# Kernel optimization log

Hardware: AMD Instinct MI355X
Metric: run time of the kernel (lower is better)

Reference implementation:

```python
import jax, jax.numpy as jnp
import numpy as np

D = 768
B = 32
N = 768


def setup_inputs() -> dict:
    key = jax.random.key(0)
    k1, k2, k3, k4 = jax.random.split(key, 4)
    stdv = 1.0 / np.sqrt(D)
    X = jax.random.normal(k1, (B, N, D), dtype=jnp.float32)
    adj = jax.random.uniform(k2, (B, N, N), dtype=jnp.float32)
    W_l = jax.random.uniform(k3, (D, D), dtype=jnp.float32, minval=-stdv, maxval=stdv)
    W_l1 = jax.random.uniform(k4, (D, D), dtype=jnp.float32, minval=-stdv, maxval=stdv)
    return {"X": X, "adj": adj, "W_l": W_l, "W_l1": W_l1}


def _row_normalize(adj):
    # rowsum^-1 with inf -> 0 (rows summing to zero stay zero)
    rowsum = adj.sum(axis=-1, keepdims=True)  # [B, N, 1]
    r_inv = jnp.where(rowsum == 0, 0.0, 1.0 / rowsum)
    return adj * r_inv


def reference(X, adj, W_l, W_l1):
    # X: [B, N, D], adj: [B, N, N]
    adj_n = _row_normalize(adj)
    e1 = jnp.einsum('bnd,de->bne', X, W_l1)        # message transform
    e11 = jnp.einsum('bnm,bmd->bnd', adj_n, e1)    # aggregate
    X1 = jnp.einsum('bnd,de->bne', X, W_l)         # self transform
    h = X1 + e11
    return jax.nn.leaky_relu(h, negative_slope=0.01)
```

## Files before the change

kernel.cpp:

```cpp
#include <hip/hip_runtime.h>
#include <hip/hip_bf16.h>
#include <cstdint>
#include <cstddef>

#define BN_ROWS 24576
#define DD 768
#define BE (768*768)
#define BM 384
#define BN_T 192
#define BK 32
#define ABUF 24576
#define BUFSZ 36864

typedef __attribute__((ext_vector_type(8))) short bf16x8;
typedef __attribute__((ext_vector_type(4))) float f32x4;

static __device__ __forceinline__ unsigned short f2bf(float f) {
  unsigned int u = __builtin_bit_cast(unsigned int, f);
  unsigned int lsb = (u >> 16) & 1u;
  u += 0x7fffu + lsb;
  return (unsigned short)(u >> 16);
}


__global__ __launch_bounds__(256) void convertX(const float* __restrict__ x,
                                                unsigned short* __restrict__ xb, int n4) {
  int idx = blockIdx.x * blockDim.x + threadIdx.x;
  int stride = gridDim.x * blockDim.x;
  for (int i = idx; i < n4; i += stride) {
    float4 v = reinterpret_cast<const float4*>(x)[i];
    ushort4 o;
    o.x = f2bf(v.x); o.y = f2bf(v.y); o.z = f2bf(v.z); o.w = f2bf(v.w);
    reinterpret_cast<ushort4*>(xb)[i] = o;
  }
}

__global__ __launch_bounds__(256) void convertWT(const float* __restrict__ Wl,
                                                 const float* __restrict__ Wl1,
                                                 unsigned short* __restrict__ WlT,
                                                 unsigned short* __restrict__ Wl1T) {
  __shared__ float tile[64][65];
  int tr = blockIdx.x / 12, tc = blockIdx.x % 12;
  int c = threadIdx.x & 63, r0 = threadIdx.x >> 6;
  const float* srcs[2] = {Wl, Wl1};
  unsigned short* dsts[2] = {WlT, Wl1T};
  #pragma unroll
  for (int m = 0; m < 2; ++m) {
    const float* src = srcs[m];
    #pragma unroll
    for (int i = 0; i < 16; ++i) {
      int r = r0 + i * 4;
      tile[r][c] = src[(size_t)(tr * 64 + r) * DD + tc * 64 + c];
    }
    __syncthreads();
    unsigned short* dst = dsts[m];
    #pragma unroll
    for (int i = 0; i < 16; ++i) {
      int r2 = r0 + i * 4;
      dst[(size_t)(tc * 64 + r2) * DD + tr * 64 + c] = f2bf(tile[c][r2]);
    }
    __syncthreads();
  }
}

__global__ __launch_bounds__(256) void adjNorm(const float* __restrict__ adj,
                                               unsigned short* __restrict__ adjnb) {
  int wid = threadIdx.x >> 6, lane = threadIdx.x & 63;
  int row = blockIdx.x * 4 + wid;
  const float4* a = reinterpret_cast<const float4*>(adj + (size_t)row * DD);
  float4 v[3];
  float s = 0.f;
  #pragma unroll
  for (int i = 0; i < 3; ++i) {
    v[i] = a[i * 64 + lane];
    s += (v[i].x + v[i].y) + (v[i].z + v[i].w);
  }
  #pragma unroll
  for (int off = 32; off; off >>= 1) s += __shfl_down(s, off);
  s = __shfl(s, 0);
  float rinv = (s == 0.f) ? 0.f : 1.f / s;
  ushort4* o = reinterpret_cast<ushort4*>(adjnb + (size_t)row * DD);
  #pragma unroll
  for (int i = 0; i < 3; ++i) {
    ushort4 u;
    u.x = f2bf(v[i].x * rinv); u.y = f2bf(v[i].y * rinv);
    u.z = f2bf(v[i].z * rinv); u.w = f2bf(v[i].w * rinv);
    o[i * 64 + lane] = u;
  }
}


template<int MODE>
__global__ __launch_bounds__(512, 2) void gemm8(
    const unsigned short* __restrict__ P0,
    const unsigned short* __restrict__ P1,
    const unsigned short* __restrict__ P2,
    const unsigned short* __restrict__ P3,
    void* __restrict__ outp)
{
  __shared__ char smem[3 * BUFSZ];
  constexpr int NT = MODE ? 48 : 24;
  const int tid = threadIdx.x, lane = tid & 63;
  const int wid = tid >> 6, wr = wid >> 1, wc = wid & 1;

  const int logical = (blockIdx.x & 7) * 32 + (blockIdx.x >> 3);

  const unsigned short *Ab0, *Bb0, *Ab1 = nullptr, *Bb1 = nullptr;
  int mt, nt, b;
  if (MODE == 0) {
    mt = logical >> 2; nt = logical & 3;
    b = mt >> 1;
    Ab0 = P0 + (size_t)mt * BM * DD;
    Bb0 = P1 + (size_t)nt * BN_T * DD;
  } else {
    b = logical >> 3; int r = logical & 7; mt = r >> 2; nt = r & 3;
    size_t bo = (size_t)b * BE;
    Ab0 = P0 + bo + (size_t)mt * BM * DD;
    Bb0 = P1 + bo + (size_t)nt * BN_T * DD;
    Ab1 = P2 + bo + (size_t)mt * BM * DD;
    Bb1 = P3 + (size_t)nt * BN_T * DD;
  }

  const int r_in = lane >> 2;
  const int s_in = lane & 3;

  auto stage = [&](int s) {
    int sc = s < NT ? s : 0;
    const int buf = (s % 3) * BUFSZ;
    const unsigned short *Abase, *Bbase;
    int kk;
    if (MODE == 1 && sc >= 24) { kk = sc - 24; Abase = Ab1; Bbase = Bb1; }
    else                       { kk = sc;      Abase = Ab0; Bbase = Bb0; }
    if (wid < 4) {
      #pragma unroll
      for (int i = 0; i < 6; ++i) {
        int row = wid * 96 + i * 16 + r_in;
        int slot = s_in ^ ((row >> 1) & 3);
        const unsigned short* src = Abase + (size_t)row * DD + kk * BK + slot * 8;
        __builtin_amdgcn_global_load_lds(
            (const __attribute__((address_space(1))) void*)src,
            (__attribute__((address_space(3))) void*)(smem + buf + (wid * 96 + i * 16) * 64),
            16, 0, 0);
      }
    } else {
      #pragma unroll
      for (int i = 0; i < 3; ++i) {
        int row = (wid - 4) * 48 + i * 16 + r_in;
        int slot = s_in ^ ((row >> 1) & 3);
        const unsigned short* src = Bbase + (size_t)row * DD + kk * BK + slot * 8;
        __builtin_amdgcn_global_load_lds(
            (const __attribute__((address_space(1))) void*)src,
            (__attribute__((address_space(3))) void*)(smem + buf + ABUF + ((wid - 4) * 48 + i * 16) * 64),
            16, 0, 0);
      }
    }
  };

  const int ks = lane >> 4;
  auto frag = [&](int off, int row) -> bf16x8 {
    int slot = ks ^ ((row >> 1) & 3);
    return *reinterpret_cast<const bf16x8*>(smem + off + row * 64 + slot * 16);
  };

  f32x4 acc[6][6] = {};

  stage(0); stage(1);

  for (int t = 0; t < NT; ++t) {
    stage(t + 2);
    if (wid < 4) asm volatile("s_waitcnt vmcnt(12)" ::: "memory");
    else         asm volatile("s_waitcnt vmcnt(6)"  ::: "memory");
    __builtin_amdgcn_s_barrier();

    const int bufA = (t % 3) * BUFSZ;
    const int bufB = bufA + ABUF;
    bf16x8 af[6], bg[6];
    #pragma unroll
    for (int i = 0; i < 6; ++i) {
      af[i] = frag(bufA, wr * 96 + i * 16 + (lane & 15));
      bg[i] = frag(bufB, wc * 96 + i * 16 + (lane & 15));
    }
    __builtin_amdgcn_s_setprio(1);
    #pragma unroll
    for (int mi = 0; mi < 6; ++mi)
      #pragma unroll
      for (int ni = 0; ni < 6; ++ni)
        acc[mi][ni] = __builtin_amdgcn_mfma_f32_16x16x32_bf16(af[mi], bg[ni], acc[mi][ni], 0, 0, 0);
    __builtin_amdgcn_s_setprio(0);
    __builtin_amdgcn_s_barrier();
  }

  if (MODE == 0) {
    unsigned short* ob = (unsigned short*)outp + (size_t)b * BE;
    const int mloc = (mt & 1) * BM + wr * 96 + (lane >> 4) * 4;
    #pragma unroll
    for (int mi = 0; mi < 6; ++mi)
      #pragma unroll
      for (int ni = 0; ni < 6; ++ni) {
        int m = mloc + mi * 16;
        int d = nt * BN_T + wc * 96 + ni * 16 + (lane & 15);
        f32x4 v = acc[mi][ni];
        ushort4 o;
        o.x = f2bf(v[0]); o.y = f2bf(v[1]); o.z = f2bf(v[2]); o.w = f2bf(v[3]);
        *reinterpret_cast<ushort4*>(ob + (size_t)d * DD + m) = o;
      }
  } else {
    float* ob = (float*)outp + (size_t)b * BE;
    const int mloc = mt * BM + wr * 96 + (lane >> 4) * 4;
    #pragma unroll
    for (int mi = 0; mi < 6; ++mi)
      #pragma unroll
      for (int ni = 0; ni < 6; ++ni) {
        int m = mloc + mi * 16;
        int n = nt * BN_T + wc * 96 + ni * 16 + (lane & 15);
        f32x4 v = acc[mi][ni];
        #pragma unroll
        for (int j = 0; j < 4; ++j) {
          float x = v[j];
          ob[(size_t)(m + j) * DD + n] = x > 0.f ? x : 0.01f * x;
        }
      }
  }
}


extern "C" void kernel_launch(void* const* d_in, const int* in_sizes, int n_in,
                              void* d_out, int out_size, void* d_ws, size_t ws_size,
                              hipStream_t stream) {
  const float* X   = (const float*)d_in[0];
  const float* adj = (const float*)d_in[1];
  const float* Wl  = (const float*)d_in[2];
  const float* Wl1 = (const float*)d_in[3];
  float* out = (float*)d_out;

  char* ws = (char*)d_ws;
  const size_t SZ = (size_t)BN_ROWS * DD * 2;
  unsigned short* Xb    = (unsigned short*)(ws);
  unsigned short* adjnb = (unsigned short*)(ws + SZ);
  unsigned short* e1T   = (unsigned short*)(ws + 2 * SZ);
  unsigned short* WlT   = (unsigned short*)(ws + 3 * SZ);
  unsigned short* Wl1T  = (unsigned short*)(ws + 3 * SZ + (size_t)BE * 2);

  convertX<<<4096, 256, 0, stream>>>(X, Xb, (BN_ROWS * DD) / 4);
  convertWT<<<144, 256, 0, stream>>>(Wl, Wl1, WlT, Wl1T);
  adjNorm<<<BN_ROWS / 4, 256, 0, stream>>>(adj, adjnb);
  gemm8<0><<<256, 512, 0, stream>>>(Xb, Wl1T, nullptr, nullptr, e1T);
  gemm8<1><<<256, 512, 0, stream>>>(adjnb, e1T, Xb, WlT, out);
}
```

Before: 156.0 us.

## Use 12-wave GEMM blocks with 4x3 warp grid and reordered prefetch pipeline

Raises the GEMM block from 8 to 12 waves, arranged as a 4x3 warp grid with 96x64 sub-tiles, so every wave issues three async global-to-LDS loads per stage instead of the earlier uneven A/B split. The loop now takes one barrier per iteration, reads the fragments first, then issues the next stage's prefetch before the MFMAs. It waits on vmcnt(3) at the end of each iteration. The goal is more waves per block to hide latency and less barrier overhead. The cost is fewer accumulators per wave, more LDS fragment reads in total, and occupancy limited to one 768-thread block per CU.

```diff
diff --git a/kernel.cpp b/kernel.cpp
--- a/kernel.cpp
+++ b/kernel.cpp
@@ -91,7 +91,7 @@
 
 
 template<int MODE>
-__global__ __launch_bounds__(512, 2) void gemm8(
+__global__ __launch_bounds__(768) void gemm12(
     const unsigned short* __restrict__ P0,
     const unsigned short* __restrict__ P1,
     const unsigned short* __restrict__ P2,
@@ -101,7 +101,9 @@
   __shared__ char smem[3 * BUFSZ];
   constexpr int NT = MODE ? 48 : 24;
   const int tid = threadIdx.x, lane = tid & 63;
-  const int wid = tid >> 6, wr = wid >> 1, wc = wid & 1;
+  const int wid = tid >> 6;
+  const int wr = wid & 3;
+  const int wc = wid >> 2;
 
   const int logical = (blockIdx.x & 7) * 32 + (blockIdx.x >> 3);
 
@@ -121,38 +123,28 @@
     Bb1 = P3 + (size_t)nt * BN_T * DD;
   }
 
+  const bool isA = wid < 8;
+  const int chunk0 = isA ? wid * 3 : (wid - 8) * 3;
+  const int ldsbase0 = (isA ? 0 : ABUF) + chunk0 * 1024;
   const int r_in = lane >> 2;
   const int s_in = lane & 3;
 
   auto stage = [&](int s) {
     int sc = s < NT ? s : 0;
     const int buf = (s % 3) * BUFSZ;
-    const unsigned short *Abase, *Bbase;
+    const unsigned short* base;
     int kk;
-    if (MODE == 1 && sc >= 24) { kk = sc - 24; Abase = Ab1; Bbase = Bb1; }
-    else                       { kk = sc;      Abase = Ab0; Bbase = Bb0; }
-    if (wid < 4) {
-      #pragma unroll
-      for (int i = 0; i < 6; ++i) {
-        int row = wid * 96 + i * 16 + r_in;
-        int slot = s_in ^ ((row >> 1) & 3);
-        const unsigned short* src = Abase + (size_t)row * DD + kk * BK + slot * 8;
-        __builtin_amdgcn_global_load_lds(
-            (const __attribute__((address_space(1))) void*)src,
-            (__attribute__((address_space(3))) void*)(smem + buf + (wid * 96 + i * 16) * 64),
-            16, 0, 0);
-      }
-    } else {
-      #pragma unroll
-      for (int i = 0; i < 3; ++i) {
-        int row = (wid - 4) * 48 + i * 16 + r_in;
-        int slot = s_in ^ ((row >> 1) & 3);
-        const unsigned short* src = Bbase + (size_t)row * DD + kk * BK + slot * 8;
-        __builtin_amdgcn_global_load_lds(
-            (const __attribute__((address_space(1))) void*)src,
-            (__attribute__((address_space(3))) void*)(smem + buf + ABUF + ((wid - 4) * 48 + i * 16) * 64),
-            16, 0, 0);
-      }
+    if (MODE == 1 && sc >= 24) { kk = sc - 24; base = isA ? Ab1 : Bb1; }
+    else                       { kk = sc;      base = isA ? Ab0 : Bb0; }
+    #pragma unroll
+    for (int i = 0; i < 3; ++i) {
+      int row = (chunk0 + i) * 16 + r_in;
+      int slot = s_in ^ ((row >> 1) & 3);
+      const unsigned short* src = base + (size_t)row * DD + kk * BK + slot * 8;
+      __builtin_amdgcn_global_load_lds(
+          (const __attribute__((address_space(1))) void*)src,
+          (__attribute__((address_space(3))) void*)(smem + buf + ldsbase0 + i * 1024),
+          16, 0, 0);
     }
   };
 
@@ -162,32 +154,41 @@
     return *reinterpret_cast<const bf16x8*>(smem + off + row * 64 + slot * 16);
   };
 
-  f32x4 acc[6][6] = {};
+  f32x4 acc[6][4] = {};
 
   stage(0); stage(1);
+  asm volatile("s_waitcnt vmcnt(3)" ::: "memory");
+
+  const int arow = wr * 96 + (lane & 15);
+  const int brow = wc * 64 + (lane & 15);
 
   for (int t = 0; t < NT; ++t) {
-    stage(t + 2);
-    if (wid < 4) asm volatile("s_waitcnt vmcnt(12)" ::: "memory");
-    else         asm volatile("s_waitcnt vmcnt(6)"  ::: "memory");
     __builtin_amdgcn_s_barrier();
-
     const int bufA = (t % 3) * BUFSZ;
     const int bufB = bufA + ABUF;
-    bf16x8 af[6], bg[6];
-    #pragma unroll
-    for (int i = 0; i < 6; ++i) {
-      af[i] = frag(bufA, wr * 96 + i * 16 + (lane & 15));
-      bg[i] = frag(bufB, wc * 96 + i * 16 + (lane & 15));
-    }
+
+    bf16x8 a[6], bg[4];
+    #pragma unroll
+    for (int i = 0; i < 6; ++i) a[i] = frag(bufA, arow + i * 16);
+    #pragma unroll
+    for (int i = 0; i < 4; ++i) bg[i] = frag(bufB, brow + i * 16);
+
+    stage(t + 2);
+
     __builtin_amdgcn_s_setprio(1);
     #pragma unroll
-    for (int mi = 0; mi < 6; ++mi)
-      #pragma unroll
-      for (int ni = 0; ni < 6; ++ni)
-        acc[mi][ni] = __builtin_amdgcn_mfma_f32_16x16x32_bf16(af[mi], bg[ni], acc[mi][ni], 0, 0, 0);
+    for (int ni = 0; ni < 2; ++ni)
+      #pragma unroll
+      for (int mi = 0; mi < 6; ++mi)
+        acc[mi][ni] = __builtin_amdgcn_mfma_f32_16x16x32_bf16(a[mi], bg[ni], acc[mi][ni], 0, 0, 0);
+    #pragma unroll
+    for (int ni = 2; ni < 4; ++ni)
+      #pragma unroll
+      for (int mi = 0; mi < 6; ++mi)
+        acc[mi][ni] = __builtin_amdgcn_mfma_f32_16x16x32_bf16(a[mi], bg[ni], acc[mi][ni], 0, 0, 0);
     __builtin_amdgcn_s_setprio(0);
-    __builtin_amdgcn_s_barrier();
+
+    asm volatile("s_waitcnt vmcnt(3)" ::: "memory");
   }
 
   if (MODE == 0) {
@@ -196,9 +197,9 @@
     #pragma unroll
     for (int mi = 0; mi < 6; ++mi)
       #pragma unroll
-      for (int ni = 0; ni < 6; ++ni) {
+      for (int ni = 0; ni < 4; ++ni) {
         int m = mloc + mi * 16;
-        int d = nt * BN_T + wc * 96 + ni * 16 + (lane & 15);
+        int d = nt * BN_T + wc * 64 + ni * 16 + (lane & 15);
         f32x4 v = acc[mi][ni];
         ushort4 o;
         o.x = f2bf(v[0]); o.y = f2bf(v[1]); o.z = f2bf(v[2]); o.w = f2bf(v[3]);
@@ -210,9 +211,9 @@
     #pragma unroll
     for (int mi = 0; mi < 6; ++mi)
       #pragma unroll
-      for (int ni = 0; ni < 6; ++ni) {
+      for (int ni = 0; ni < 4; ++ni) {
         int m = mloc + mi * 16;
-        int n = nt * BN_T + wc * 96 + ni * 16 + (lane & 15);
+        int n = nt * BN_T + wc * 64 + ni * 16 + (lane & 15);
         f32x4 v = acc[mi][ni];
         #pragma unroll
         for (int j = 0; j < 4; ++j) {
@@ -244,6 +245,6 @@
   convertX<<<4096, 256, 0, stream>>>(X, Xb, (BN_ROWS * DD) / 4);
   convertWT<<<144, 256, 0, stream>>>(Wl, Wl1, WlT, Wl1T);
   adjNorm<<<BN_ROWS / 4, 256, 0, stream>>>(adj, adjnb);
-  gemm8<0><<<256, 512, 0, stream>>>(Xb, Wl1T, nullptr, nullptr, e1T);
-  gemm8<1><<<256, 512, 0, stream>>>(adjnb, e1T, Xb, WlT, out);
-}
+  gemm12<0><<<256, 768, 0, stream>>>(Xb, Wl1T, nullptr, nullptr, e1T);
+  gemm12<1><<<256, 768, 0, stream>>>(adjnb, e1T, Xb, WlT, out);
+}
```

New measurement: 186.7 us. +19.7%, slower.

## Shrink GEMM tiles to 192x192 with 4 waves and double-buffered LDS

Applied to the files above, without the earlier changes.

Halves the M tile to 192 and drops each GEMM block from 8 waves to 4, so the grid doubles to 512 blocks. The LDS pipeline goes from three buffers with a two-stage prefetch to two buffers. The next stage's load is now issued after the fragment reads, with a full vmcnt(0) wait and a single barrier per iteration. The goal is better CU occupancy and load balance across 256 CUs, at the cost of less prefetch depth and more B-tile re-reads from global memory.

```diff
diff --git a/kernel.cpp b/kernel.cpp
--- a/kernel.cpp
+++ b/kernel.cpp
@@ -6,11 +6,11 @@
 #define BN_ROWS 24576
 #define DD 768
 #define BE (768*768)
-#define BM 384
+#define BM 192
 #define BN_T 192
 #define BK 32
-#define ABUF 24576
-#define BUFSZ 36864
+#define ABUF 12288
+#define BUFSZ 24576
 
 typedef __attribute__((ext_vector_type(8))) short bf16x8;
 typedef __attribute__((ext_vector_type(4))) float f32x4;
@@ -91,29 +91,30 @@
 
 
 template<int MODE>
-__global__ __launch_bounds__(512, 2) void gemm8(
+__global__ __launch_bounds__(256, 2) void gemm4(
     const unsigned short* __restrict__ P0,
     const unsigned short* __restrict__ P1,
     const unsigned short* __restrict__ P2,
     const unsigned short* __restrict__ P3,
     void* __restrict__ outp)
 {
-  __shared__ char smem[3 * BUFSZ];
+  __shared__ char smem[2 * BUFSZ];
   constexpr int NT = MODE ? 48 : 24;
   const int tid = threadIdx.x, lane = tid & 63;
-  const int wid = tid >> 6, wr = wid >> 1, wc = wid & 1;
-
-  const int logical = (blockIdx.x & 7) * 32 + (blockIdx.x >> 3);
+  const int wid = tid >> 6;
+  const int wr = wid >> 1, wc = wid & 1;
+
+  const int logical = (blockIdx.x & 7) * 64 + (blockIdx.x >> 3);
 
   const unsigned short *Ab0, *Bb0, *Ab1 = nullptr, *Bb1 = nullptr;
   int mt, nt, b;
   if (MODE == 0) {
     mt = logical >> 2; nt = logical & 3;
-    b = mt >> 1;
+    b = mt >> 2;
     Ab0 = P0 + (size_t)mt * BM * DD;
     Bb0 = P1 + (size_t)nt * BN_T * DD;
   } else {
-    b = logical >> 3; int r = logical & 7; mt = r >> 2; nt = r & 3;
+    b = logical >> 4; int r = logical & 15; mt = r >> 2; nt = r & 3;
     size_t bo = (size_t)b * BE;
     Ab0 = P0 + bo + (size_t)mt * BM * DD;
     Bb0 = P1 + bo + (size_t)nt * BN_T * DD;
@@ -125,34 +126,23 @@
   const int s_in = lane & 3;
 
   auto stage = [&](int s) {
-    int sc = s < NT ? s : 0;
-    const int buf = (s % 3) * BUFSZ;
-    const unsigned short *Abase, *Bbase;
+    const int buf = (s & 1) * BUFSZ;
+    const unsigned short *Ab, *Bb;
     int kk;
-    if (MODE == 1 && sc >= 24) { kk = sc - 24; Abase = Ab1; Bbase = Bb1; }
-    else                       { kk = sc;      Abase = Ab0; Bbase = Bb0; }
-    if (wid < 4) {
-      #pragma unroll
-      for (int i = 0; i < 6; ++i) {
-        int row = wid * 96 + i * 16 + r_in;
-        int slot = s_in ^ ((row >> 1) & 3);
-        const unsigned short* src = Abase + (size_t)row * DD + kk * BK + slot * 8;
-        __builtin_amdgcn_global_load_lds(
-            (const __attribute__((address_space(1))) void*)src,
-            (__attribute__((address_space(3))) void*)(smem + buf + (wid * 96 + i * 16) * 64),
-            16, 0, 0);
-      }
-    } else {
-      #pragma unroll
-      for (int i = 0; i < 3; ++i) {
-        int row = (wid - 4) * 48 + i * 16 + r_in;
-        int slot = s_in ^ ((row >> 1) & 3);
-        const unsigned short* src = Bbase + (size_t)row * DD + kk * BK + slot * 8;
-        __builtin_amdgcn_global_load_lds(
-            (const __attribute__((address_space(1))) void*)src,
-            (__attribute__((address_space(3))) void*)(smem + buf + ABUF + ((wid - 4) * 48 + i * 16) * 64),
-            16, 0, 0);
-      }
+    if (MODE == 1 && s >= 24) { kk = s - 24; Ab = Ab1; Bb = Bb1; }
+    else                      { kk = s;      Ab = Ab0; Bb = Bb0; }
+    #pragma unroll
+    for (int i = 0; i < 6; ++i) {
+      int chunk = wid * 6 + i;
+      bool isA = chunk < 12;
+      int c = isA ? chunk : chunk - 12;
+      int row = c * 16 + r_in;
+      int slot = s_in ^ ((row >> 1) & 3);
+      const unsigned short* src = (isA ? Ab : Bb) + (size_t)row * DD + kk * BK + slot * 8;
+      __builtin_amdgcn_global_load_lds(
+          (const __attribute__((address_space(1))) void*)src,
+          (__attribute__((address_space(3))) void*)(smem + buf + (isA ? 0 : ABUF) + c * 1024),
+          16, 0, 0);
     }
   };
 
@@ -163,36 +153,37 @@
   };
 
   f32x4 acc[6][6] = {};
-
-  stage(0); stage(1);
+  const int arow = wr * 96 + (lane & 15);
+  const int brow = wc * 96 + (lane & 15);
+
+  stage(0);
 
   for (int t = 0; t < NT; ++t) {
-    stage(t + 2);
-    if (wid < 4) asm volatile("s_waitcnt vmcnt(12)" ::: "memory");
-    else         asm volatile("s_waitcnt vmcnt(6)"  ::: "memory");
+    asm volatile("s_waitcnt vmcnt(0)" ::: "memory");
     __builtin_amdgcn_s_barrier();
 
-    const int bufA = (t % 3) * BUFSZ;
+    const int bufA = (t & 1) * BUFSZ;
     const int bufB = bufA + ABUF;
-    bf16x8 af[6], bg[6];
-    #pragma unroll
-    for (int i = 0; i < 6; ++i) {
-      af[i] = frag(bufA, wr * 96 + i * 16 + (lane & 15));
-      bg[i] = frag(bufB, wc * 96 + i * 16 + (lane & 15));
-    }
+    bf16x8 a[6], bg[6];
+    #pragma unroll
+    for (int i = 0; i < 6; ++i) a[i] = frag(bufA, arow + i * 16);
+    #pragma unroll
+    for (int i = 0; i < 6; ++i) bg[i] = frag(bufB, brow + i * 16);
+
+    if (t + 1 < NT) stage(t + 1);
+
     __builtin_amdgcn_s_setprio(1);
     #pragma unroll
     for (int mi = 0; mi < 6; ++mi)
       #pragma unroll
       for (int ni = 0; ni < 6; ++ni)
-        acc[mi][ni] = __builtin_amdgcn_mfma_f32_16x16x32_bf16(af[mi], bg[ni], acc[mi][ni], 0, 0, 0);
+        acc[mi][ni] = __builtin_amdgcn_mfma_f32_16x16x32_bf16(a[mi], bg[ni], acc[mi][ni], 0, 0, 0);
     __builtin_amdgcn_s_setprio(0);
-    __builtin_amdgcn_s_barrier();
   }
 
   if (MODE == 0) {
     unsigned short* ob = (unsigned short*)outp + (size_t)b * BE;
-    const int mloc = (mt & 1) * BM + wr * 96 + (lane >> 4) * 4;
+    const int mloc = (mt & 3) * BM + wr * 96 + (lane >> 4) * 4;
     #pragma unroll
     for (int mi = 0; mi < 6; ++mi)
       #pragma unroll
@@ -244,6 +235,6 @@
   convertX<<<4096, 256, 0, stream>>>(X, Xb, (BN_ROWS * DD) / 4);
   convertWT<<<144, 256, 0, stream>>>(Wl, Wl1, WlT, Wl1T);
   adjNorm<<<BN_ROWS / 4, 256, 0, stream>>>(adj, adjnb);
-  gemm8<0><<<256, 512, 0, stream>>>(Xb, Wl1T, nullptr, nullptr, e1T);
-  gemm8<1><<<256, 512, 0, stream>>>(adjnb, e1T, Xb, WlT, out);
-}
+  gemm4<0><<<512, 256, 0, stream>>>(Xb, Wl1T, nullptr, nullptr, e1T);
+  gemm4<1><<<512, 256, 0, stream>>>(adjnb, e1T, Xb, WlT, out);
+}
```

New measurement: 152.0 us. -2.6%, faster.
